# Performance work log

Hardware: AMD Instinct MI355X
Metric: run time of the kernel (lower is better)

Reference implementation:

```python
import jax, jax.numpy as jnp
import numpy as np

# FP4 E2M1 lookup: sign bit in nibble bit 3, values {0,.5,1,1.5,2,3,4,6}
FP4_VALUES = jnp.array([0.0, 0.5, 1.0, 1.5, 2.0, 3.0, 4.0, 6.0,
                        -0.0, -0.5, -1.0, -1.5, -2.0, -3.0, -4.0, -6.0],
                       dtype=jnp.float32)
BLOCK = 32  # MX block size: one E8M0 scale per 32 elements along K
E8M0_BIAS = 127.0


def _dequant_mxfp4(packed, scales):
    """packed: [R, K//2] int bytes (two fp4 nibbles each, low nibble first).
    scales: [R, K//32] float32 biased E8M0 exponents. Returns [R, K] float32."""
    lo = packed & 0xF
    hi = (packed >> 4) & 0xF
    idx = jnp.stack([lo, hi], axis=-1).reshape(packed.shape[0], -1)  # [R, K]
    vals = FP4_VALUES[idx]                                           # [R, K]
    R, K = vals.shape
    scale = jnp.exp2(scales - E8M0_BIAS)                             # [R, K//32]
    vals = vals.reshape(R, K // BLOCK, BLOCK) * scale[..., None]
    return vals.reshape(R, K)


def setup_inputs() -> dict:
    key = jax.random.key(0)
    k1, k2, k3, k4 = jax.random.split(key, 4)
    M = N = 4096
    K = 4096
    a = jax.random.randint(k1, (M, K // 2), 0, 256, dtype=jnp.int32)
    b = jax.random.randint(k2, (N, K // 2), 0, 256, dtype=jnp.int32)
    scales_a = jax.random.randint(k3, (M, K // BLOCK), 120, 132).astype(jnp.float32)
    scales_b = jax.random.randint(k4, (N, K // BLOCK), 120, 132).astype(jnp.float32)
    return {"a": a, "b": b, "scales_a": scales_a, "scales_b": scales_b}


def reference(a, b, scales_a, scales_b):
    a_f = _dequant_mxfp4(a, scales_a)          # [M, K]
    b_f = _dequant_mxfp4(b, scales_b)          # [N, K]
    return jnp.einsum('mk,nk->mn', a_f, b_f)   # [M, N]
```

## Files before the change

### kernel.cpp

```cpp
#include <hip/hip_runtime.h>
#include <hip/hip_bf16.h>
#include <stdint.h>

typedef __attribute__((ext_vector_type(4))) int   i32x4;
typedef __attribute__((ext_vector_type(8))) int   i32x8;
typedef __attribute__((ext_vector_type(4))) float f32x4;
typedef __attribute__((ext_vector_type(2))) unsigned int u32x2;

#define MDIM   4096
#define NDIM   4096
#define KBYTES 2048
#define NKBLK  128

#define BM   256
#define BN   256
#define BKB  128
#define KT   (KBYTES / BKB)

#define BARF()  asm volatile("s_barrier" ::: "memory")
#define LGKM0() asm volatile("s_waitcnt lgkmcnt(0)" ::: "memory")
#define VM0()   asm volatile("s_waitcnt vmcnt(0)" ::: "memory")

__global__ void repack_bytes(const int* __restrict__ a, const int* __restrict__ b,
                             uint32_t* __restrict__ ap, uint32_t* __restrict__ bp) {
  const size_t n4 = (size_t)MDIM * KBYTES / 4;
  for (size_t i = (size_t)blockIdx.x * blockDim.x + threadIdx.x; i < n4;
       i += (size_t)gridDim.x * blockDim.x) {
    i32x4 va = *(const i32x4*)(a + i * 4);
    ap[i] = (uint32_t)(va.x & 255) | ((uint32_t)(va.y & 255) << 8) |
            ((uint32_t)(va.z & 255) << 16) | ((uint32_t)(va.w & 255) << 24);
    i32x4 vb = *(const i32x4*)(b + i * 4);
    bp[i] = (uint32_t)(vb.x & 255) | ((uint32_t)(vb.y & 255) << 8) |
            ((uint32_t)(vb.z & 255) << 16) | ((uint32_t)(vb.w & 255) << 24);
  }
}

__global__ void repack_scales(const float* __restrict__ sa, const float* __restrict__ sb,
                              uint8_t* __restrict__ sat, uint8_t* __restrict__ sbt) {
  int t = blockIdx.x * blockDim.x + threadIdx.x;
  if (t >= MDIM * NKBLK) return;
  int m  = t >> 7;
  int kb = t & 127;
  int o  = kb * 4096 + (m & 15) * 256 + (m >> 4);
  sat[o] = (uint8_t)(int)sa[t];
  sbt[o] = (uint8_t)(int)sb[t];
}

__device__ __forceinline__ i32x8 frag8(i32x4 v) {
  i32x8 r = {v.x, v.y, v.z, v.w, 0, 0, 0, 0};
  return r;
}

__device__ __forceinline__ int sbyte2(u32x2 p, int i) {
  return (int)((i < 4 ? (p.x >> (i * 8)) : (p.y >> ((i - 4) * 8))) & 0xffu);
}

__global__ __launch_bounds__(512, 2) void mxfp4_gemm(
    const uint8_t* __restrict__ ap, const uint8_t* __restrict__ bp,
    const uint8_t* __restrict__ sat, const uint8_t* __restrict__ sbt,
    float* __restrict__ out) {
  extern __shared__ uint8_t lds[];

  const int tid  = threadIdx.x;
  const int lane = tid & 63;
  const int w    = tid >> 6;
  const int wrow = w >> 2;
  const int wcol = w & 3;
  const int g    = lane >> 4;
  const int l15  = lane & 15;
  const int lx   = l15 & 7;

  const int bx = blockIdx.x;
  const int by = blockIdx.y;

  const uint8_t* aBase = ap + (size_t)(by * BM) * KBYTES;
  const uint8_t* bBase = bp + (size_t)(bx * BN) * KBYTES;

  const int srow  = lane >> 3;
  const int sslot = (lane & 7) ^ srow;
  const int soff  = srow * KBYTES + sslot * 16;
  const int arow0 = w * 32;

  const uint8_t* sAp = sat + (size_t)l15 * 256 + by * 16 + wrow * 8;
  const uint8_t* sBp = sbt + (size_t)l15 * 256 + bx * 16 + wcol * 4;

#define STAGE_A(dstbase, kt1, c)                                                         \
  __builtin_amdgcn_global_load_lds(                                                      \
      (__attribute__((address_space(1))) void*)(aBase + (size_t)(arow0 + (c) * 8) * KBYTES + (kt1) * BKB + soff), \
      (__attribute__((address_space(3))) void*)((dstbase) + (arow0 + (c) * 8) * 128), 16, 0, 0)
#define STAGE_B(dstbase, kt1, c)                                                         \
  __builtin_amdgcn_global_load_lds(                                                      \
      (__attribute__((address_space(1))) void*)(bBase + (size_t)(arow0 + (c) * 8) * KBYTES + (kt1) * BKB + soff), \
      (__attribute__((address_space(3))) void*)((dstbase) + 32768 + (arow0 + (c) * 8) * 128), 16, 0, 0)

  f32x4 acc[8][4] = {};
  i32x4 a0[4], a1[4], bf[4];
  u32x2 sAc0, sAc1, sAn0, sAn1;
  uint32_t sBc0, sBc1, sBn0, sBn1;

  {
    uint8_t* d = lds;
#pragma unroll
    for (int c = 0; c < 4; ++c) { STAGE_A(d, 0, c); STAGE_B(d, 0, c); }
    sAc0 = *(const u32x2*)(sAp + (size_t)(0 + g) * 4096);
    sAc1 = *(const u32x2*)(sAp + (size_t)(4 + g) * 4096);
    sBc0 = *(const uint32_t*)(sBp + (size_t)(0 + g) * 4096);
    sBc1 = *(const uint32_t*)(sBp + (size_t)(4 + g) * 4096);
    VM0();
    BARF();
  }

  for (int kt = 0; kt < KT; ++kt) {
    const int cur = kt & 1;
    uint8_t* cA = lds + cur * 65536;
    uint8_t* cB = cA + 32768;
    uint8_t* nD = lds + (cur ^ 1) * 65536;
    const bool pf = (kt + 1 < KT);

#pragma unroll
    for (int ns = 0; ns < 4; ++ns)
      bf[ns] = *(const i32x4*)(cB + (wcol * 64 + ns * 16 + l15) * 128 + ((0 + g) ^ lx) * 16);
#pragma unroll
    for (int ms = 0; ms < 4; ++ms)
      a0[ms] = *(const i32x4*)(cA + (wrow * 128 + ms * 16 + l15) * 128 + ((0 + g) ^ lx) * 16);
    if (pf) {
#pragma unroll
      for (int c = 0; c < 4; ++c) STAGE_A(nD, kt + 1, c);
    }
    BARF();
    LGKM0();
    __builtin_amdgcn_s_setprio(1);
#pragma unroll
    for (int ms = 0; ms < 4; ++ms) {
      const int sa = sbyte2(sAc0, ms);
#pragma unroll
      for (int ns = 0; ns < 4; ++ns)
        acc[ms][ns] = __builtin_amdgcn_mfma_scale_f32_16x16x128_f8f6f4(
            frag8(a0[ms]), frag8(bf[ns]), acc[ms][ns], 4, 4,
            0, sa, 0, (int)((sBc0 >> (ns * 8)) & 0xffu));
    }
    __builtin_amdgcn_s_setprio(0);
    BARF();

#pragma unroll
    for (int ms = 0; ms < 4; ++ms)
      a1[ms] = *(const i32x4*)(cA + (wrow * 128 + (ms + 4) * 16 + l15) * 128 + ((0 + g) ^ lx) * 16);
    if (pf) {
#pragma unroll
      for (int c = 0; c < 4; ++c) STAGE_B(nD, kt + 1, c);
      sAn0 = *(const u32x2*)(sAp + (size_t)((kt + 1) * 8 + 0 + g) * 4096);
      sAn1 = *(const u32x2*)(sAp + (size_t)((kt + 1) * 8 + 4 + g) * 4096);
      sBn0 = *(const uint32_t*)(sBp + (size_t)((kt + 1) * 8 + 0 + g) * 4096);
      sBn1 = *(const uint32_t*)(sBp + (size_t)((kt + 1) * 8 + 4 + g) * 4096);
    }
    BARF();
    LGKM0();
    __builtin_amdgcn_s_setprio(1);
#pragma unroll
    for (int ms = 0; ms < 4; ++ms) {
      const int sa = sbyte2(sAc0, ms + 4);
#pragma unroll
      for (int ns = 0; ns < 4; ++ns)
        acc[ms + 4][ns] = __builtin_amdgcn_mfma_scale_f32_16x16x128_f8f6f4(
            frag8(a1[ms]), frag8(bf[ns]), acc[ms + 4][ns], 4, 4,
            0, sa, 0, (int)((sBc0 >> (ns * 8)) & 0xffu));
    }
    __builtin_amdgcn_s_setprio(0);
    BARF();

#pragma unroll
    for (int ns = 0; ns < 4; ++ns)
      bf[ns] = *(const i32x4*)(cB + (wcol * 64 + ns * 16 + l15) * 128 + ((4 + g) ^ lx) * 16);
#pragma unroll
    for (int ms = 0; ms < 4; ++ms)
      a0[ms] = *(const i32x4*)(cA + (wrow * 128 + ms * 16 + l15) * 128 + ((4 + g) ^ lx) * 16);
    BARF();
    LGKM0();
    __builtin_amdgcn_s_setprio(1);
#pragma unroll
    for (int ms = 0; ms < 4; ++ms) {
      const int sa = sbyte2(sAc1, ms);
#pragma unroll
      for (int ns = 0; ns < 4; ++ns)
        acc[ms][ns] = __builtin_amdgcn_mfma_scale_f32_16x16x128_f8f6f4(
            frag8(a0[ms]), frag8(bf[ns]), acc[ms][ns], 4, 4,
            0, sa, 0, (int)((sBc1 >> (ns * 8)) & 0xffu));
    }
    __builtin_amdgcn_s_setprio(0);
    BARF();

#pragma unroll
    for (int ms = 0; ms < 4; ++ms)
      a1[ms] = *(const i32x4*)(cA + (wrow * 128 + (ms + 4) * 16 + l15) * 128 + ((4 + g) ^ lx) * 16);
    BARF();
    LGKM0();
    __builtin_amdgcn_s_setprio(1);
#pragma unroll
    for (int ms = 0; ms < 4; ++ms) {
      const int sa = sbyte2(sAc1, ms + 4);
#pragma unroll
      for (int ns = 0; ns < 4; ++ns)
        acc[ms + 4][ns] = __builtin_amdgcn_mfma_scale_f32_16x16x128_f8f6f4(
            frag8(a1[ms]), frag8(bf[ns]), acc[ms + 4][ns], 4, 4,
            0, sa, 0, (int)((sBc1 >> (ns * 8)) & 0xffu));
    }
    __builtin_amdgcn_s_setprio(0);
    sAc0 = sAn0; sAc1 = sAn1; sBc0 = sBn0; sBc1 = sBn1;
    VM0();
    BARF();
  }

  float* ob = out + (size_t)(by * BM + wrow * 128) * NDIM + bx * BN + wcol * 64;
#pragma unroll
  for (int ms = 0; ms < 8; ++ms)
#pragma unroll
    for (int ns = 0; ns < 4; ++ns) {
#pragma unroll
      for (int r = 0; r < 4; ++r)
        ob[(size_t)(ms * 16 + g * 4 + r) * NDIM + ns * 16 + l15] = acc[ms][ns][r];
    }
#undef STAGE_A
#undef STAGE_B
}

extern "C" void kernel_launch(void* const* d_in, const int* in_sizes, int n_in,
                              void* d_out, int out_size, void* d_ws, size_t ws_size,
                              hipStream_t stream) {
  (void)in_sizes; (void)n_in; (void)out_size; (void)ws_size;
  const int*   a  = (const int*)d_in[0];
  const int*   b  = (const int*)d_in[1];
  const float* sa = (const float*)d_in[2];
  const float* sb = (const float*)d_in[3];
  float* out = (float*)d_out;

  uint8_t* ws = (uint8_t*)d_ws;
  uint32_t* ap = (uint32_t*)ws;
  uint32_t* bp = (uint32_t*)(ws + (8u << 20));
  uint8_t*  sat = ws + (16u << 20);
  uint8_t*  sbt = ws + (16u << 20) + (512u << 10);

  repack_bytes<<<2048, 256, 0, stream>>>(a, b, ap, bp);
  repack_scales<<<(MDIM * NKBLK + 255) / 256, 256, 0, stream>>>(sa, sb, sat, sbt);

  hipFuncSetAttribute((const void*)mxfp4_gemm,
                      hipFuncAttributeMaxDynamicSharedMemorySize, 131072);

  dim3 grid(NDIM / BN, MDIM / BM);
  mxfp4_gemm<<<grid, 512, 131072, stream>>>((const uint8_t*)ap, (const uint8_t*)bp,
                                            sat, sbt, out);
}
```

Before: 79.91 us.

## Split LDS tiles into K-half planes and deepen prefetch with partial vmcnt waits

The LDS layout changes from 128-byte rows to two 64-byte K-half planes per matrix, with a new XOR swizzle for both staging and reads. Global-to-LDS staging is now issued per K-half, running up to two half-tiles ahead. The end-of-iteration wait becomes vmcnt(6) instead of a full drain, so memory loads stay in flight across iterations. The wrapped prefetch indices (kt+1, kt+2 mod KT) issue redundant loads on the final iterations, and correctness now relies on the exact vmcnt accounting.

```diff
diff --git a/kernel.cpp b/kernel.cpp
--- a/kernel.cpp
+++ b/kernel.cpp
@@ -19,7 +19,7 @@
 
 #define BARF()  asm volatile("s_barrier" ::: "memory")
 #define LGKM0() asm volatile("s_waitcnt lgkmcnt(0)" ::: "memory")
-#define VM0()   asm volatile("s_waitcnt vmcnt(0)" ::: "memory")
+#define VMC6()  asm volatile("s_waitcnt vmcnt(6)" ::: "memory")
 
 __global__ void repack_bytes(const int* __restrict__ a, const int* __restrict__ b,
                              uint32_t* __restrict__ ap, uint32_t* __restrict__ bp) {
@@ -68,7 +68,6 @@
   const int wcol = w & 3;
   const int g    = lane >> 4;
   const int l15  = lane & 15;
-  const int lx   = l15 & 7;
 
   const int bx = blockIdx.x;
   const int by = blockIdx.y;
@@ -76,137 +75,144 @@
   const uint8_t* aBase = ap + (size_t)(by * BM) * KBYTES;
   const uint8_t* bBase = bp + (size_t)(bx * BN) * KBYTES;
 
-  const int srow  = lane >> 3;
-  const int sslot = (lane & 7) ^ srow;
-  const int soff  = srow * KBYTES + sslot * 16;
+  const int rdslot = (g ^ ((l15 >> 1) & 3)) * 16;
+  const int sr = lane >> 2, sp = lane & 3;
+  const int soff4 = sr * KBYTES + ((sp ^ ((sr >> 1) & 3)) * 16);
   const int arow0 = w * 32;
+
+#define PLANE(bufi, mat, kwX) (lds + (bufi) * 65536 + (mat) * 32768 + (kwX) * 16384)
+
+#define STAGE_HALF(bufi, ktX, kwX)                                                        \
+  do {                                                                                    \
+    const uint8_t* _sa = aBase + (size_t)arow0 * KBYTES + (ktX) * BKB + (kwX) * 64 + soff4; \
+    const uint8_t* _sb = bBase + (size_t)arow0 * KBYTES + (ktX) * BKB + (kwX) * 64 + soff4; \
+    uint8_t* _da = PLANE(bufi, 0, kwX) + arow0 * 64;                                      \
+    uint8_t* _db = PLANE(bufi, 1, kwX) + arow0 * 64;                                      \
+    __builtin_amdgcn_global_load_lds((__attribute__((address_space(1))) void*)_sa,        \
+        (__attribute__((address_space(3))) void*)_da, 16, 0, 0);                          \
+    __builtin_amdgcn_global_load_lds((__attribute__((address_space(1))) void*)(_sa + 16 * KBYTES), \
+        (__attribute__((address_space(3))) void*)(_da + 1024), 16, 0, 0);                 \
+    __builtin_amdgcn_global_load_lds((__attribute__((address_space(1))) void*)_sb,        \
+        (__attribute__((address_space(3))) void*)(_db), 16, 0, 0);                        \
+    __builtin_amdgcn_global_load_lds((__attribute__((address_space(1))) void*)(_sb + 16 * KBYTES), \
+        (__attribute__((address_space(3))) void*)(_db + 1024), 16, 0, 0);                 \
+  } while (0)
 
   const uint8_t* sAp = sat + (size_t)l15 * 256 + by * 16 + wrow * 8;
   const uint8_t* sBp = sbt + (size_t)l15 * 256 + bx * 16 + wcol * 4;
 
-#define STAGE_A(dstbase, kt1, c)                                                         \
-  __builtin_amdgcn_global_load_lds(                                                      \
-      (__attribute__((address_space(1))) void*)(aBase + (size_t)(arow0 + (c) * 8) * KBYTES + (kt1) * BKB + soff), \
-      (__attribute__((address_space(3))) void*)((dstbase) + (arow0 + (c) * 8) * 128), 16, 0, 0)
-#define STAGE_B(dstbase, kt1, c)                                                         \
-  __builtin_amdgcn_global_load_lds(                                                      \
-      (__attribute__((address_space(1))) void*)(bBase + (size_t)(arow0 + (c) * 8) * KBYTES + (kt1) * BKB + soff), \
-      (__attribute__((address_space(3))) void*)((dstbase) + 32768 + (arow0 + (c) * 8) * 128), 16, 0, 0)
-
   f32x4 acc[8][4] = {};
   i32x4 a0[4], a1[4], bf[4];
-  u32x2 sAc0, sAc1, sAn0, sAn1;
-  uint32_t sBc0, sBc1, sBn0, sBn1;
-
-  {
-    uint8_t* d = lds;
-#pragma unroll
-    for (int c = 0; c < 4; ++c) { STAGE_A(d, 0, c); STAGE_B(d, 0, c); }
-    sAc0 = *(const u32x2*)(sAp + (size_t)(0 + g) * 4096);
-    sAc1 = *(const u32x2*)(sAp + (size_t)(4 + g) * 4096);
-    sBc0 = *(const uint32_t*)(sBp + (size_t)(0 + g) * 4096);
-    sBc1 = *(const uint32_t*)(sBp + (size_t)(4 + g) * 4096);
-    VM0();
-    BARF();
-  }
+  u32x2 sA0c, sA0m, sA0n, sA1c, sA1n;
+  uint32_t sB0c, sB0m, sB0n, sB1c, sB1n;
+
+  STAGE_HALF(0, 0, 0);
+  sA0c = *(const u32x2*)(sAp + (size_t)(0 * 8 + 0 + g) * 4096);
+  sB0c = *(const uint32_t*)(sBp + (size_t)(0 * 8 + 0 + g) * 4096);
+  STAGE_HALF(0, 0, 1);
+  sA1c = *(const u32x2*)(sAp + (size_t)(0 * 8 + 4 + g) * 4096);
+  sB1c = *(const uint32_t*)(sBp + (size_t)(0 * 8 + 4 + g) * 4096);
+  STAGE_HALF(1, 1, 0);
+  sA0m = *(const u32x2*)(sAp + (size_t)(1 * 8 + 0 + g) * 4096);
+  sB0m = *(const uint32_t*)(sBp + (size_t)(1 * 8 + 0 + g) * 4096);
+  VMC6();
+  BARF();
 
   for (int kt = 0; kt < KT; ++kt) {
     const int cur = kt & 1;
-    uint8_t* cA = lds + cur * 65536;
-    uint8_t* cB = cA + 32768;
-    uint8_t* nD = lds + (cur ^ 1) * 65536;
-    const bool pf = (kt + 1 < KT);
+    const int nxt = cur ^ 1;
+    const uint8_t* A0 = PLANE(cur, 0, 0);
+    const uint8_t* B0 = PLANE(cur, 1, 0);
+    const uint8_t* A1p = PLANE(cur, 0, 1);
+    const uint8_t* B1p = PLANE(cur, 1, 1);
+    const int kt1 = (kt + 1) & (KT - 1);
+    const int kt2 = (kt + 2) & (KT - 1);
 
 #pragma unroll
     for (int ns = 0; ns < 4; ++ns)
-      bf[ns] = *(const i32x4*)(cB + (wcol * 64 + ns * 16 + l15) * 128 + ((0 + g) ^ lx) * 16);
-#pragma unroll
-    for (int ms = 0; ms < 4; ++ms)
-      a0[ms] = *(const i32x4*)(cA + (wrow * 128 + ms * 16 + l15) * 128 + ((0 + g) ^ lx) * 16);
-    if (pf) {
-#pragma unroll
-      for (int c = 0; c < 4; ++c) STAGE_A(nD, kt + 1, c);
-    }
-    BARF();
-    LGKM0();
-    __builtin_amdgcn_s_setprio(1);
-#pragma unroll
-    for (int ms = 0; ms < 4; ++ms) {
-      const int sa = sbyte2(sAc0, ms);
+      bf[ns] = *(const i32x4*)(B0 + (wcol * 64 + ns * 16 + l15) * 64 + rdslot);
+#pragma unroll
+    for (int ms = 0; ms < 4; ++ms)
+      a0[ms] = *(const i32x4*)(A0 + (wrow * 128 + ms * 16 + l15) * 64 + rdslot);
+    STAGE_HALF(nxt, kt1, 1);
+    sA1n = *(const u32x2*)(sAp + (size_t)(kt1 * 8 + 4 + g) * 4096);
+    sB1n = *(const uint32_t*)(sBp + (size_t)(kt1 * 8 + 4 + g) * 4096);
+    BARF();
+    LGKM0();
+    __builtin_amdgcn_s_setprio(1);
+#pragma unroll
+    for (int ms = 0; ms < 4; ++ms) {
+      const int sa = sbyte2(sA0c, ms);
 #pragma unroll
       for (int ns = 0; ns < 4; ++ns)
         acc[ms][ns] = __builtin_amdgcn_mfma_scale_f32_16x16x128_f8f6f4(
             frag8(a0[ms]), frag8(bf[ns]), acc[ms][ns], 4, 4,
-            0, sa, 0, (int)((sBc0 >> (ns * 8)) & 0xffu));
-    }
-    __builtin_amdgcn_s_setprio(0);
-    BARF();
-
-#pragma unroll
-    for (int ms = 0; ms < 4; ++ms)
-      a1[ms] = *(const i32x4*)(cA + (wrow * 128 + (ms + 4) * 16 + l15) * 128 + ((0 + g) ^ lx) * 16);
-    if (pf) {
-#pragma unroll
-      for (int c = 0; c < 4; ++c) STAGE_B(nD, kt + 1, c);
-      sAn0 = *(const u32x2*)(sAp + (size_t)((kt + 1) * 8 + 0 + g) * 4096);
-      sAn1 = *(const u32x2*)(sAp + (size_t)((kt + 1) * 8 + 4 + g) * 4096);
-      sBn0 = *(const uint32_t*)(sBp + (size_t)((kt + 1) * 8 + 0 + g) * 4096);
-      sBn1 = *(const uint32_t*)(sBp + (size_t)((kt + 1) * 8 + 4 + g) * 4096);
-    }
-    BARF();
-    LGKM0();
-    __builtin_amdgcn_s_setprio(1);
-#pragma unroll
-    for (int ms = 0; ms < 4; ++ms) {
-      const int sa = sbyte2(sAc0, ms + 4);
+            0, sa, 0, (int)((sB0c >> (ns * 8)) & 0xffu));
+    }
+    __builtin_amdgcn_s_setprio(0);
+    BARF();
+
+#pragma unroll
+    for (int ms = 0; ms < 4; ++ms)
+      a1[ms] = *(const i32x4*)(A0 + (wrow * 128 + (ms + 4) * 16 + l15) * 64 + rdslot);
+    BARF();
+    LGKM0();
+    __builtin_amdgcn_s_setprio(1);
+#pragma unroll
+    for (int ms = 0; ms < 4; ++ms) {
+      const int sa = sbyte2(sA0c, ms + 4);
 #pragma unroll
       for (int ns = 0; ns < 4; ++ns)
         acc[ms + 4][ns] = __builtin_amdgcn_mfma_scale_f32_16x16x128_f8f6f4(
             frag8(a1[ms]), frag8(bf[ns]), acc[ms + 4][ns], 4, 4,
-            0, sa, 0, (int)((sBc0 >> (ns * 8)) & 0xffu));
+            0, sa, 0, (int)((sB0c >> (ns * 8)) & 0xffu));
     }
     __builtin_amdgcn_s_setprio(0);
     BARF();
 
 #pragma unroll
     for (int ns = 0; ns < 4; ++ns)
-      bf[ns] = *(const i32x4*)(cB + (wcol * 64 + ns * 16 + l15) * 128 + ((4 + g) ^ lx) * 16);
-#pragma unroll
-    for (int ms = 0; ms < 4; ++ms)
-      a0[ms] = *(const i32x4*)(cA + (wrow * 128 + ms * 16 + l15) * 128 + ((4 + g) ^ lx) * 16);
-    BARF();
-    LGKM0();
-    __builtin_amdgcn_s_setprio(1);
-#pragma unroll
-    for (int ms = 0; ms < 4; ++ms) {
-      const int sa = sbyte2(sAc1, ms);
+      bf[ns] = *(const i32x4*)(B1p + (wcol * 64 + ns * 16 + l15) * 64 + rdslot);
+#pragma unroll
+    for (int ms = 0; ms < 4; ++ms)
+      a0[ms] = *(const i32x4*)(A1p + (wrow * 128 + ms * 16 + l15) * 64 + rdslot);
+    STAGE_HALF(cur, kt2, 0);
+    sA0n = *(const u32x2*)(sAp + (size_t)(kt2 * 8 + 0 + g) * 4096);
+    sB0n = *(const uint32_t*)(sBp + (size_t)(kt2 * 8 + 0 + g) * 4096);
+    BARF();
+    LGKM0();
+    __builtin_amdgcn_s_setprio(1);
+#pragma unroll
+    for (int ms = 0; ms < 4; ++ms) {
+      const int sa = sbyte2(sA1c, ms);
 #pragma unroll
       for (int ns = 0; ns < 4; ++ns)
         acc[ms][ns] = __builtin_amdgcn_mfma_scale_f32_16x16x128_f8f6f4(
             frag8(a0[ms]), frag8(bf[ns]), acc[ms][ns], 4, 4,
-            0, sa, 0, (int)((sBc1 >> (ns * 8)) & 0xffu));
-    }
-    __builtin_amdgcn_s_setprio(0);
-    BARF();
-
-#pragma unroll
-    for (int ms = 0; ms < 4; ++ms)
-      a1[ms] = *(const i32x4*)(cA + (wrow * 128 + (ms + 4) * 16 + l15) * 128 + ((4 + g) ^ lx) * 16);
-    BARF();
-    LGKM0();
-    __builtin_amdgcn_s_setprio(1);
-#pragma unroll
-    for (int ms = 0; ms < 4; ++ms) {
-      const int sa = sbyte2(sAc1, ms + 4);
+            0, sa, 0, (int)((sB1c >> (ns * 8)) & 0xffu));
+    }
+    __builtin_amdgcn_s_setprio(0);
+    BARF();
+
+#pragma unroll
+    for (int ms = 0; ms < 4; ++ms)
+      a1[ms] = *(const i32x4*)(A1p + (wrow * 128 + (ms + 4) * 16 + l15) * 64 + rdslot);
+    BARF();
+    LGKM0();
+    __builtin_amdgcn_s_setprio(1);
+#pragma unroll
+    for (int ms = 0; ms < 4; ++ms) {
+      const int sa = sbyte2(sA1c, ms + 4);
 #pragma unroll
       for (int ns = 0; ns < 4; ++ns)
         acc[ms + 4][ns] = __builtin_amdgcn_mfma_scale_f32_16x16x128_f8f6f4(
             frag8(a1[ms]), frag8(bf[ns]), acc[ms + 4][ns], 4, 4,
-            0, sa, 0, (int)((sBc1 >> (ns * 8)) & 0xffu));
-    }
-    __builtin_amdgcn_s_setprio(0);
-    sAc0 = sAn0; sAc1 = sAn1; sBc0 = sBn0; sBc1 = sBn1;
-    VM0();
+            0, sa, 0, (int)((sB1c >> (ns * 8)) & 0xffu));
+    }
+    __builtin_amdgcn_s_setprio(0);
+    sA0c = sA0m; sB0c = sB0m; sA0m = sA0n; sB0m = sB0n;
+    sA1c = sA1n; sB1c = sB1n;
+    VMC6();
     BARF();
   }
 
@@ -219,8 +225,8 @@
       for (int r = 0; r < 4; ++r)
         ob[(size_t)(ms * 16 + g * 4 + r) * NDIM + ns * 16 + l15] = acc[ms][ns][r];
     }
-#undef STAGE_A
-#undef STAGE_B
+#undef STAGE_HALF
+#undef PLANE
 }
 
 extern "C" void kernel_launch(void* const* d_in, const int* in_sizes, int n_in,
```

New measurement: 83.56 us. +4.6%, slower.
